# Kernel tuning notes

Hardware: AMD Instinct MI355X
Metric: run time of the kernel (lower is better)

## Reference

```python
import jax, jax.numpy as jnp
import numpy as np

M_PER_GROUP = 16
EPS = 0.001


def setup_inputs() -> dict:
    key = jax.random.key(0)
    x = jax.random.normal(key, (32, 64, 64, 256), dtype=jnp.float32)
    return {"x": x}


def reference(x) -> jnp.ndarray:
    # x: [B, W, H, C] (NHWC). Training-phase path, decomposition='cholesky', renorm=False.
    b, w, h, c = x.shape
    groups = c // M_PER_GROUP
    n = b * w * h  # samples per channel

    # [C, B*W*H]
    x_flat = jnp.transpose(x, (3, 0, 1, 2)).reshape(c, -1)
    mean = jnp.mean(x_flat, axis=1, keepdims=True)          # [C, 1]
    f = x_flat - mean                                        # [C, N]

    # per-group covariance: [G, m, N] -> [G, m, m]
    fg = f.reshape(groups, M_PER_GROUP, -1)
    denom = jnp.float32(n) - 1.0
    cov = jnp.einsum('gmn,gkn->gmk', fg, fg) / denom
    eye = jnp.eye(M_PER_GROUP, dtype=x.dtype)
    cov = (1.0 - EPS) * cov + EPS * eye
    # NOTE: the original TF code divides by (N-1) a second time after shrinkage;
    # reproduced faithfully here.
    cov = cov / denom

    # batched Cholesky + triangular solve: inv_sqrt = L^{-1}
    chol = jnp.linalg.cholesky(cov)                          # [G, m, m], lower
    inv_sqrt = jax.vmap(
        lambda L: jax.scipy.linalg.solve_triangular(L, eye, lower=True)
    )(chol)                                                  # [G, m, m]

    # whiten: [G, m, m] @ [G, m, N] -> [G, m, N]
    f_hat = jnp.einsum('gmk,gkn->gmn', inv_sqrt, fg)
    out = f_hat.reshape(c, b, w, h)
    return jnp.transpose(out, (1, 2, 3, 0))
```

## Files before the change

### kernel.cpp

```cpp
#include <hip/hip_runtime.h>


#define NROWS   131072
#define DENOMF  131071.0f
#define EPSV    0.001f

#define OFF_INV    0
#define OFF_BIAS   4096
#define OFF_RED1   4352
#define OFF_PART4  217344
#define GSTATS     13312

typedef __attribute__((ext_vector_type(8))) short bf16x8;
typedef __attribute__((ext_vector_type(4))) float f32x4;
typedef __attribute__((ext_vector_type(4))) unsigned int u32x4;

__device__ __forceinline__ unsigned int fbits(float v) {
    return __builtin_bit_cast(unsigned int, v);
}
__device__ __forceinline__ float bfloat(unsigned int u) {
    return __builtin_bit_cast(float, u);
}

struct Row8 { float a, b, c, d, e, f, g, h; };

__device__ __forceinline__ void cvt8(const Row8 r, bf16x8& hv, bf16x8& lv, float& s) {
    s += ((r.a + r.b) + (r.c + r.d)) + ((r.e + r.f) + (r.g + r.h));
    const unsigned int ua = fbits(r.a), ub = fbits(r.b), uc = fbits(r.c), ud = fbits(r.d);
    const unsigned int ue = fbits(r.e), uf = fbits(r.f), ug = fbits(r.g), uh = fbits(r.h);
    u32x4 hp;
    hp.x = (ub & 0xFFFF0000u) | (ua >> 16);
    hp.y = (ud & 0xFFFF0000u) | (uc >> 16);
    hp.z = (uf & 0xFFFF0000u) | (ue >> 16);
    hp.w = (uh & 0xFFFF0000u) | (ug >> 16);
    const float da = r.a - bfloat(ua & 0xFFFF0000u);
    const float db = r.b - bfloat(ub & 0xFFFF0000u);
    const float dc = r.c - bfloat(uc & 0xFFFF0000u);
    const float dd = r.d - bfloat(ud & 0xFFFF0000u);
    const float de = r.e - bfloat(ue & 0xFFFF0000u);
    const float df = r.f - bfloat(uf & 0xFFFF0000u);
    const float dg = r.g - bfloat(ug & 0xFFFF0000u);
    const float dh = r.h - bfloat(uh & 0xFFFF0000u);
    u32x4 lp;
    lp.x = (fbits(db) & 0xFFFF0000u) | (fbits(da) >> 16);
    lp.y = (fbits(dd) & 0xFFFF0000u) | (fbits(dc) >> 16);
    lp.z = (fbits(df) & 0xFFFF0000u) | (fbits(de) >> 16);
    lp.w = (fbits(dh) & 0xFFFF0000u) | (fbits(dg) >> 16);
    hv = __builtin_bit_cast(bf16x8, hp);
    lv = __builtin_bit_cast(bf16x8, lp);
}

__global__ __launch_bounds__(256, 2) void k1_stats(const float* __restrict__ x,
                                                   float* __restrict__ ws, int NB) {
    __shared__ float xt[32 * 260];
    const int tid = threadIdx.x;
    const int lane = tid & 63, wv = tid >> 6;
    const int slot = lane >> 4;
    const int TPB = (NROWS / 32) / NB;
    const float4* gf4 = reinterpret_cast<const float4*>(x);
    const size_t tile0 = (size_t)blockIdx.x * TPB;

    const int rb = wv * 64 + (lane & 15);
    const int ro0 = (slot * 8 + ((0 + 2 * slot) & 7)) * 260 + rb;
    const int ro1 = (slot * 8 + ((1 + 2 * slot) & 7)) * 260 + rb;
    const int ro2 = (slot * 8 + ((2 + 2 * slot) & 7)) * 260 + rb;
    const int ro3 = (slot * 8 + ((3 + 2 * slot) & 7)) * 260 + rb;
    const int ro4 = (slot * 8 + ((4 + 2 * slot) & 7)) * 260 + rb;
    const int ro5 = (slot * 8 + ((5 + 2 * slot) & 7)) * 260 + rb;
    const int ro6 = (slot * 8 + ((6 + 2 * slot) & 7)) * 260 + rb;
    const int ro7 = (slot * 8 + ((7 + 2 * slot) & 7)) * 260 + rb;

    f32x4 hh0 = {0,0,0,0}, hl0 = {0,0,0,0}, ll0 = {0,0,0,0};
    f32x4 hh1 = {0,0,0,0}, hl1 = {0,0,0,0}, ll1 = {0,0,0,0};
    f32x4 hh2 = {0,0,0,0}, hl2 = {0,0,0,0}, ll2 = {0,0,0,0};
    f32x4 hh3 = {0,0,0,0}, hl3 = {0,0,0,0}, ll3 = {0,0,0,0};
    float s0 = 0.f, s1 = 0.f, s2 = 0.f, s3 = 0.f;

    float4 st0, st1, st2, st3, st4, st5, st6, st7;
#define LOADT(T)                                                              \
    {                                                                         \
        const float4* tp = gf4 + (tile0 + (T)) * 2048 + tid;                  \
        st0 = tp[0];    st1 = tp[256];  st2 = tp[512];  st3 = tp[768];        \
        st4 = tp[1024]; st5 = tp[1280]; st6 = tp[1536]; st7 = tp[1792];       \
    }
#define WRK(K, ST)                                                            \
    {                                                                         \
        const int idx = tid + (K) * 256;                                      \
        *reinterpret_cast<float4*>(&xt[(idx >> 6) * 260 + (idx & 63) * 4]) = ST; \
    }
#define PROCG(G, AHH, AHL, ALL, S)                                            \
    {                                                                         \
        Row8 r;                                                               \
        r.a = xt[ro0 + (G) * 16]; r.b = xt[ro1 + (G) * 16];                   \
        r.c = xt[ro2 + (G) * 16]; r.d = xt[ro3 + (G) * 16];                   \
        r.e = xt[ro4 + (G) * 16]; r.f = xt[ro5 + (G) * 16];                   \
        r.g = xt[ro6 + (G) * 16]; r.h = xt[ro7 + (G) * 16];                   \
        bf16x8 hv, lv;                                                        \
        cvt8(r, hv, lv, S);                                                   \
        AHH = __builtin_amdgcn_mfma_f32_16x16x32_bf16(hv, hv, AHH, 0, 0, 0);  \
        AHL = __builtin_amdgcn_mfma_f32_16x16x32_bf16(hv, lv, AHL, 0, 0, 0);  \
        ALL = __builtin_amdgcn_mfma_f32_16x16x32_bf16(lv, lv, ALL, 0, 0, 0);  \
    }

    LOADT(0);
    for (int t = 0; t < TPB; ++t) {
        __syncthreads();
        WRK(0, st0); WRK(1, st1); WRK(2, st2); WRK(3, st3);
        WRK(4, st4); WRK(5, st5); WRK(6, st6); WRK(7, st7);
        __syncthreads();
        const int tn = (t + 1 < TPB) ? (t + 1) : t;
        LOADT(tn);
        PROCG(0, hh0, hl0, ll0, s0);
        PROCG(1, hh1, hl1, ll1, s1);
        PROCG(2, hh2, hl2, ll2, s2);
        PROCG(3, hh3, hl3, ll3, s3);
    }
#undef PROCG
#undef WRK
#undef LOADT

    float* pb = ws + OFF_PART4 + (size_t)blockIdx.x * GSTATS + (size_t)(wv * 4) * 832;
#define STG(G, AHH, AHL, ALL, S)                                              \
    {                                                                         \
        float* pw = pb + (G) * 832;                                           \
        pw[0 * 64 + lane]  = AHH[0]; pw[1 * 64 + lane]  = AHH[1];             \
        pw[2 * 64 + lane]  = AHH[2]; pw[3 * 64 + lane]  = AHH[3];             \
        pw[4 * 64 + lane]  = AHL[0]; pw[5 * 64 + lane]  = AHL[1];             \
        pw[6 * 64 + lane]  = AHL[2]; pw[7 * 64 + lane]  = AHL[3];             \
        pw[8 * 64 + lane]  = ALL[0]; pw[9 * 64 + lane]  = ALL[1];             \
        pw[10 * 64 + lane] = ALL[2]; pw[11 * 64 + lane] = ALL[3];             \
        pw[12 * 64 + lane] = S;                                               \
    }
    STG(0, hh0, hl0, ll0, s0);
    STG(1, hh1, hl1, ll1, s1);
    STG(2, hh2, hl2, ll2, s2);
    STG(3, hh3, hl3, ll3, s3);
#undef STG
}

__global__ __launch_bounds__(256, 4) void k2_reduce(float* __restrict__ ws, int NB) {
    const int t = blockIdx.x * 256 + threadIdx.x;
    if (t >= GSTATS) return;
    const int per = NB / 16;
    const float* p = ws + OFF_PART4 + (size_t)(blockIdx.y * per) * GSTATS + t;
    float sum = 0.f;
#pragma unroll 8
    for (int b = 0; b < per; ++b) sum += p[(size_t)b * GSTATS];
    ws[OFF_RED1 + (size_t)blockIdx.y * GSTATS + t] = sum;
}

__global__ void k2_chol(float* __restrict__ ws, int NB) {
    __shared__ float sg[832];
    const int g = blockIdx.x, tid = threadIdx.x;

    for (int e = tid; e < 832; e += 64) {
        float v = 0.f;
#pragma unroll
        for (int y = 0; y < 16; ++y)
            v += ws[OFF_RED1 + (size_t)y * GSTATS + g * 832 + e];
        sg[e] = v;
    }
    __syncthreads();

    const int ii = tid & 15;
    const float inv_denom = 1.0f / DENOMF;
    const float cs_ii = sg[768 + ii] + sg[768 + 16 + ii] +
                        sg[768 + 32 + ii] + sg[768 + 48 + ii];
    const float mu_l = cs_ii * (1.0f / (float)NROWS);

#define GIDX(T, I, J) ((T) * 256 + ((I) & 3) * 64 + ((((I) >> 2)) << 4) + (J))
    float arow[16];
#pragma unroll
    for (int kk = 0; kk < 16; ++kk) {
        float G = sg[GIDX(0, ii, kk)] + sg[GIDX(1, ii, kk)] +
                  sg[GIDX(1, kk, ii)] + sg[GIDX(2, ii, kk)];
        float mu_k = __shfl(mu_l, kk, 64);
        float cv = (G - (float)NROWS * mu_l * mu_k) * inv_denom;
        cv = cv * (1.0f - EPSV) + ((kk == ii) ? EPSV : 0.0f);
        arow[kk] = cv * inv_denom;
    }
#undef GIDX

    float lrow[16];
#pragma unroll
    for (int j = 0; j < 16; ++j) {
        float diag = __shfl(arow[j], j, 64);
        float ljj  = sqrtf(diag);
        float lij  = (ii == j) ? ljj : arow[j] / ljj;
        lrow[j] = lij;
#pragma unroll
        for (int k = j + 1; k < 16; ++k) {
            float lkj = __shfl(lij, k, 64);
            arow[k] = fmaf(-lij, lkj, arow[k]);
        }
    }

    float xcol[16];
#pragma unroll
    for (int i2 = 0; i2 < 16; ++i2) {
        float ssum = (ii == i2) ? 1.0f : 0.0f;
#pragma unroll
        for (int k = 0; k < 16; ++k) {
            if (k < i2) {
                float Lik = __shfl(lrow[k], i2, 64);
                ssum = fmaf(-Lik, xcol[k], ssum);
            }
        }
        float Lii = __shfl(lrow[i2], i2, 64);
        xcol[i2] = (i2 >= ii) ? ssum / Lii : 0.0f;
    }

    float* invg = ws + OFF_INV + g * 256;
#pragma unroll
    for (int i2 = 0; i2 < 16; ++i2) {
        if (tid < 16) invg[i2 * 16 + tid] = xcol[i2];
        float bi = xcol[i2] * mu_l;
        bi += __shfl_xor(bi, 1, 64);
        bi += __shfl_xor(bi, 2, 64);
        bi += __shfl_xor(bi, 4, 64);
        bi += __shfl_xor(bi, 8, 64);
        if (tid == 0) ws[OFF_BIAS + g * 16 + i2] = bi;
    }
}

template <int CTRL>
__device__ __forceinline__ float dpp1(float v) {
    int iv = __builtin_bit_cast(int, v);
    int r = __builtin_amdgcn_update_dpp(iv, iv, CTRL, 0xF, 0xF, false);
    return __builtin_bit_cast(float, r);
}
template <int CTRL>
__device__ __forceinline__ float4 dpp4(float4 v) {
    float4 r;
    r.x = dpp1<CTRL>(v.x);
    r.y = dpp1<CTRL>(v.y);
    r.z = dpp1<CTRL>(v.z);
    r.w = dpp1<CTRL>(v.w);
    return r;
}

#define DOT4(O, A, V) \
    O = fmaf(A.x, V.x, O); O = fmaf(A.y, V.y, O); \
    O = fmaf(A.z, V.z, O); O = fmaf(A.w, V.w, O)

__global__ __launch_bounds__(256, 4) void k3_apply(const float* __restrict__ x,
                                                   const float* __restrict__ ws,
                                                   float* __restrict__ out) {
    const int tid = threadIdx.x, lane = tid & 63, wv = tid >> 6;
    const int q = lane & 3, g = lane >> 2;

    const float* invg = ws + OFF_INV + g * 256;
#define LOADIR(R, M) \
    *reinterpret_cast<const float4*>(invg + (4 * q + (R)) * 16 + 4 * (q ^ (M)))
    float4 ir00 = LOADIR(0, 0), ir01 = LOADIR(0, 1), ir02 = LOADIR(0, 2), ir03 = LOADIR(0, 3);
    float4 ir10 = LOADIR(1, 0), ir11 = LOADIR(1, 1), ir12 = LOADIR(1, 2), ir13 = LOADIR(1, 3);
    float4 ir20 = LOADIR(2, 0), ir21 = LOADIR(2, 1), ir22 = LOADIR(2, 2), ir23 = LOADIR(2, 3);
    float4 ir30 = LOADIR(3, 0), ir31 = LOADIR(3, 1), ir32 = LOADIR(3, 2), ir33 = LOADIR(3, 3);
#undef LOADIR
    float4 b4 = *reinterpret_cast<const float4*>(ws + OFF_BIAS + g * 16 + 4 * q);

    const int rpb   = NROWS / gridDim.x;
    const int iters = rpb / 4;
    const size_t rowbase = (size_t)blockIdx.x * rpb;
    const float4* xp = reinterpret_cast<const float4*>(x) + rowbase * 64 + lane;
    float4*       op = reinterpret_cast<float4*>(out)     + rowbase * 64 + lane;

    float4 cur = xp[(size_t)wv * 64];
    for (int i = 0; i < iters; ++i) {
        const int ip = (i + 1 < iters) ? (i + 1) : (iters - 1);
        float4 nxt = xp[(size_t)(ip * 4 + wv) * 64];

        float4 v0 = cur;
        float4 v1 = dpp4<0xB1>(cur);
        float4 v2 = dpp4<0x4E>(cur);
        float4 v3 = dpp4<0x1B>(cur);

        float o0 = -b4.x, o1 = -b4.y, o2 = -b4.z, o3 = -b4.w;
        DOT4(o0, ir00, v0); DOT4(o0, ir01, v1); DOT4(o0, ir02, v2); DOT4(o0, ir03, v3);
        DOT4(o1, ir10, v0); DOT4(o1, ir11, v1); DOT4(o1, ir12, v2); DOT4(o1, ir13, v3);
        DOT4(o2, ir20, v0); DOT4(o2, ir21, v1); DOT4(o2, ir22, v2); DOT4(o2, ir23, v3);
        DOT4(o3, ir30, v0); DOT4(o3, ir31, v1); DOT4(o3, ir32, v2); DOT4(o3, ir33, v3);

        op[(size_t)(i * 4 + wv) * 64] = make_float4(o0, o1, o2, o3);
        cur = nxt;
    }
}

extern "C" void kernel_launch(void* const* d_in, const int* in_sizes, int n_in,
                              void* d_out, int out_size, void* d_ws, size_t ws_size,
                              hipStream_t stream) {
    const float* x = (const float*)d_in[0];
    float* out = (float*)d_out;
    float* ws  = (float*)d_ws;

    int NB = 128;
    if (ws_size >= (size_t)(OFF_PART4 + 512 * GSTATS) * sizeof(float)) NB = 512;
    else if (ws_size >= (size_t)(OFF_PART4 + 256 * GSTATS) * sizeof(float)) NB = 256;

    k1_stats<<<NB, 256, 0, stream>>>(x, ws, NB);
    dim3 rg((GSTATS + 255) / 256, 16);
    k2_reduce<<<rg, 256, 0, stream>>>(ws, NB);
    k2_chol<<<16, 64, 0, stream>>>(ws, NB);
    k3_apply<<<1024, 256, 0, stream>>>(x, ws, out);
}
```

Baseline: 98.80 us.

## Double-buffer stats tile with direct global-to-LDS async loads

The covariance-stats kernel now stages each 32-row tile straight from global memory into LDS using global_load_lds, instead of loading into registers and then writing to shared memory. The shared buffer is doubled so the next tile loads while the current one is processed, and one barrier per iteration is dropped. This aims to cut register pressure and the LDS write instructions, and to overlap memory traffic with MFMA work. It doubles the LDS footprint, which may lower occupancy. Correctness depends on the async LDS writes being complete before the barrier, and it is unclear whether the compiler inserts a wait on them before __syncthreads.

New measurement: 98.46 us. Within noise of the previous version (-0.3%).

```diff
diff --git a/kernel.cpp b/kernel.cpp
--- a/kernel.cpp
+++ b/kernel.cpp
@@ -20,6 +20,12 @@
 }
 __device__ __forceinline__ float bfloat(unsigned int u) {
     return __builtin_bit_cast(float, u);
+}
+
+__device__ __forceinline__ void gload_lds16(float* lds, const float* g) {
+    __builtin_amdgcn_global_load_lds(
+        (const __attribute__((address_space(1))) unsigned int*)g,
+        (__attribute__((address_space(3))) unsigned int*)lds, 16, 0, 0);
 }
 
 struct Row8 { float a, b, c, d, e, f, g, h; };
@@ -52,12 +58,11 @@
 
 __global__ __launch_bounds__(256, 2) void k1_stats(const float* __restrict__ x,
                                                    float* __restrict__ ws, int NB) {
-    __shared__ float xt[32 * 260];
+    __shared__ float xt[2][32 * 260];
     const int tid = threadIdx.x;
     const int lane = tid & 63, wv = tid >> 6;
     const int slot = lane >> 4;
     const int TPB = (NROWS / 32) / NB;
-    const float4* gf4 = reinterpret_cast<const float4*>(x);
     const size_t tile0 = (size_t)blockIdx.x * TPB;
 
     const int rb = wv * 64 + (lane & 15);
@@ -76,60 +81,64 @@
     f32x4 hh3 = {0,0,0,0}, hl3 = {0,0,0,0}, ll3 = {0,0,0,0};
     float s0 = 0.f, s1 = 0.f, s2 = 0.f, s3 = 0.f;
 
-    float4 st0, st1, st2, st3, st4, st5, st6, st7;
-#define LOADT(T)                                                              \
+#define STAGE(B, T)                                                           \
     {                                                                         \
-        const float4* tp = gf4 + (tile0 + (T)) * 2048 + tid;                  \
-        st0 = tp[0];    st1 = tp[256];  st2 = tp[512];  st3 = tp[768];        \
-        st4 = tp[1024]; st5 = tp[1280]; st6 = tp[1536]; st7 = tp[1792];       \
-    }
-#define WRK(K, ST)                                                            \
+        const float* gp = x + ((tile0 + (T)) * 32 + (size_t)(wv * 8)) * 256   \
+                            + (size_t)lane * 4;                               \
+        float* lb = &xt[B][(wv * 8) * 260];                                   \
+        gload_lds16(lb + 0 * 260, gp + 0 * 256);                              \
+        gload_lds16(lb + 1 * 260, gp + 1 * 256);                              \
+        gload_lds16(lb + 2 * 260, gp + 2 * 256);                              \
+        gload_lds16(lb + 3 * 260, gp + 3 * 256);                              \
+        gload_lds16(lb + 4 * 260, gp + 4 * 256);                              \
+        gload_lds16(lb + 5 * 260, gp + 5 * 256);                              \
+        gload_lds16(lb + 6 * 260, gp + 6 * 256);                              \
+        gload_lds16(lb + 7 * 260, gp + 7 * 256);                              \
+    }
+#define PROCG(B, G, AHH, AHL, ALL, S)                                         \
     {                                                                         \
-        const int idx = tid + (K) * 256;                                      \
-        *reinterpret_cast<float4*>(&xt[(idx >> 6) * 260 + (idx & 63) * 4]) = ST; \
-    }
-#define PROCG(G, AHH, AHL, ALL, S)                                            \
-    {                                                                         \
+        const float* bp = &xt[B][0];                                          \
         Row8 r;                                                               \
-        r.a = xt[ro0 + (G) * 16]; r.b = xt[ro1 + (G) * 16];                   \
-        r.c = xt[ro2 + (G) * 16]; r.d = xt[ro3 + (G) * 16];                   \
-        r.e = xt[ro4 + (G) * 16]; r.f = xt[ro5 + (G) * 16];                   \
-        r.g = xt[ro6 + (G) * 16]; r.h = xt[ro7 + (G) * 16];                   \
+        r.a = bp[ro0 + (G) * 16]; r.b = bp[ro1 + (G) * 16];                   \
+        r.c = bp[ro2 + (G) * 16]; r.d = bp[ro3 + (G) * 16];                   \
+        r.e = bp[ro4 + (G) * 16]; r.f = bp[ro5 + (G) * 16];                   \
+        r.g = bp[ro6 + (G) * 16]; r.h = bp[ro7 + (G) * 16];                   \
         bf16x8 hv, lv;                                                        \
         cvt8(r, hv, lv, S);                                                   \
         AHH = __builtin_amdgcn_mfma_f32_16x16x32_bf16(hv, hv, AHH, 0, 0, 0);  \
         AHL = __builtin_amdgcn_mfma_f32_16x16x32_bf16(hv, lv, AHL, 0, 0, 0);  \
         ALL = __builtin_amdgcn_mfma_f32_16x16x32_bf16(lv, lv, ALL, 0, 0, 0);  \
     }
-
-    LOADT(0);
-    for (int t = 0; t < TPB; ++t) {
+#define PROC4(B)                                                              \
+    PROCG(B, 0, hh0, hl0, ll0, s0);                                           \
+    PROCG(B, 1, hh1, hl1, ll1, s1);                                           \
+    PROCG(B, 2, hh2, hl2, ll2, s2);                                           \
+    PROCG(B, 3, hh3, hl3, ll3, s3);
+
+    STAGE(0, 0);
+    for (int t = 0; t < TPB - 1; ++t) {
         __syncthreads();
-        WRK(0, st0); WRK(1, st1); WRK(2, st2); WRK(3, st3);
-        WRK(4, st4); WRK(5, st5); WRK(6, st6); WRK(7, st7);
-        __syncthreads();
-        const int tn = (t + 1 < TPB) ? (t + 1) : t;
-        LOADT(tn);
-        PROCG(0, hh0, hl0, ll0, s0);
-        PROCG(1, hh1, hl1, ll1, s1);
-        PROCG(2, hh2, hl2, ll2, s2);
-        PROCG(3, hh3, hl3, ll3, s3);
-    }
+        STAGE((t + 1) & 1, t + 1);
+        PROC4(t & 1);
+    }
+    __syncthreads();
+    PROC4((TPB - 1) & 1);
+#undef PROC4
 #undef PROCG
-#undef WRK
-#undef LOADT
-
+#undef STAGE
+
+    const int lane2 = lane;
     float* pb = ws + OFF_PART4 + (size_t)blockIdx.x * GSTATS + (size_t)(wv * 4) * 832;
 #define STG(G, AHH, AHL, ALL, S)                                              \
     {                                                                         \
         float* pw = pb + (G) * 832;                                           \
-        pw[0 * 64 + lane]  = AHH[0]; pw[1 * 64 + lane]  = AHH[1];             \
-        pw[2 * 64 + lane]  = AHH[2]; pw[3 * 64 + lane]  = AHH[3];             \
-        pw[4 * 64 + lane]  = AHL[0]; pw[5 * 64 + lane]  = AHL[1];             \
-        pw[6 * 64 + lane]  = AHL[2]; pw[7 * 64 + lane]  = AHL[3];             \
-        pw[8 * 64 + lane]  = ALL[0]; pw[9 * 64 + lane]  = ALL[1];             \
-        pw[10 * 64 + lane] = ALL[2]; pw[11 * 64 + lane] = ALL[3];             \
-        pw[12 * 64 + lane] = S;                                               \
+        pw[0 * 64 + lane2]  = AHH[0]; pw[1 * 64 + lane2]  = AHH[1];           \
+        pw[2 * 64 + lane2]  = AHH[2]; pw[3 * 64 + lane2]  = AHH[3];           \
+        pw[4 * 64 + lane2]  = AHL[0]; pw[5 * 64 + lane2]  = AHL[1];           \
+        pw[6 * 64 + lane2]  = AHL[2]; pw[7 * 64 + lane2]  = AHL[3];           \
+        pw[8 * 64 + lane2]  = ALL[0]; pw[9 * 64 + lane2]  = ALL[1];           \
+        pw[10 * 64 + lane2] = ALL[2]; pw[11 * 64 + lane2] = ALL[3];           \
+        pw[12 * 64 + lane2] = S;                                              \
     }
     STG(0, hh0, hl0, ll0, s0);
     STG(1, hh1, hl1, ll1, s1);
```

## Widen stats blocks to 512 threads, fold hh+ll partials, shrink partial buffers

Applied to the files above, without the earlier changes.

The stats kernel now runs 512-thread blocks over 64-row tiles. Each wave handles two channel groups across two 32-row halves instead of four groups over one half, which halves the MFMA accumulator registers per wave. The hh and ll Gram partials are summed before they are stored, so each group's partial shrinks from 832 to 576 floats and the reduce and Cholesky kernels read less data. The maximum block count drops from 512 to 256. This trades fewer, larger blocks and lower grid parallelism for less partial-sum traffic and higher occupancy per block.

New measurement: 92.97 us. -5.9%, faster.

```diff
diff --git a/kernel.cpp b/kernel.cpp
--- a/kernel.cpp
+++ b/kernel.cpp
@@ -7,9 +7,9 @@
 
 #define OFF_INV    0
 #define OFF_BIAS   4096
-#define OFF_RED1   4352
-#define OFF_PART4  217344
-#define GSTATS     13312
+#define OFF_RED    4352
+#define OFF_PART   151808
+#define GS2        9216
 
 typedef __attribute__((ext_vector_type(8))) short bf16x8;
 typedef __attribute__((ext_vector_type(4))) float f32x4;
@@ -50,51 +50,54 @@
     lv = __builtin_bit_cast(bf16x8, lp);
 }
 
-__global__ __launch_bounds__(256, 2) void k1_stats(const float* __restrict__ x,
+__global__ __launch_bounds__(512, 4) void k1_stats(const float* __restrict__ x,
                                                    float* __restrict__ ws, int NB) {
-    __shared__ float xt[32 * 260];
+    __shared__ float xt[64 * 260];
     const int tid = threadIdx.x;
     const int lane = tid & 63, wv = tid >> 6;
     const int slot = lane >> 4;
-    const int TPB = (NROWS / 32) / NB;
+    const int TPB = (NROWS / 64) / NB;
     const float4* gf4 = reinterpret_cast<const float4*>(x);
     const size_t tile0 = (size_t)blockIdx.x * TPB;
 
-    const int rb = wv * 64 + (lane & 15);
-    const int ro0 = (slot * 8 + ((0 + 2 * slot) & 7)) * 260 + rb;
-    const int ro1 = (slot * 8 + ((1 + 2 * slot) & 7)) * 260 + rb;
-    const int ro2 = (slot * 8 + ((2 + 2 * slot) & 7)) * 260 + rb;
-    const int ro3 = (slot * 8 + ((3 + 2 * slot) & 7)) * 260 + rb;
-    const int ro4 = (slot * 8 + ((4 + 2 * slot) & 7)) * 260 + rb;
-    const int ro5 = (slot * 8 + ((5 + 2 * slot) & 7)) * 260 + rb;
-    const int ro6 = (slot * 8 + ((6 + 2 * slot) & 7)) * 260 + rb;
-    const int ro7 = (slot * 8 + ((7 + 2 * slot) & 7)) * 260 + rb;
+    const int g0 = wv * 2;
+    const int rb0 = g0 * 16 + (lane & 15);
+    const int roA0 = (0 * 32 + slot * 8 + ((0 + 2 * slot) & 7)) * 260 + rb0;
+    const int roA1 = (0 * 32 + slot * 8 + ((1 + 2 * slot) & 7)) * 260 + rb0;
+    const int roA2 = (0 * 32 + slot * 8 + ((2 + 2 * slot) & 7)) * 260 + rb0;
+    const int roA3 = (0 * 32 + slot * 8 + ((3 + 2 * slot) & 7)) * 260 + rb0;
+    const int roA4 = (0 * 32 + slot * 8 + ((4 + 2 * slot) & 7)) * 260 + rb0;
+    const int roA5 = (0 * 32 + slot * 8 + ((5 + 2 * slot) & 7)) * 260 + rb0;
+    const int roA6 = (0 * 32 + slot * 8 + ((6 + 2 * slot) & 7)) * 260 + rb0;
+    const int roA7 = (0 * 32 + slot * 8 + ((7 + 2 * slot) & 7)) * 260 + rb0;
+    const int roB0 = roA0 + 32 * 260, roB1 = roA1 + 32 * 260;
+    const int roB2 = roA2 + 32 * 260, roB3 = roA3 + 32 * 260;
+    const int roB4 = roA4 + 32 * 260, roB5 = roA5 + 32 * 260;
+    const int roB6 = roA6 + 32 * 260, roB7 = roA7 + 32 * 260;
 
     f32x4 hh0 = {0,0,0,0}, hl0 = {0,0,0,0}, ll0 = {0,0,0,0};
     f32x4 hh1 = {0,0,0,0}, hl1 = {0,0,0,0}, ll1 = {0,0,0,0};
-    f32x4 hh2 = {0,0,0,0}, hl2 = {0,0,0,0}, ll2 = {0,0,0,0};
-    f32x4 hh3 = {0,0,0,0}, hl3 = {0,0,0,0}, ll3 = {0,0,0,0};
-    float s0 = 0.f, s1 = 0.f, s2 = 0.f, s3 = 0.f;
+    float s0 = 0.f, s1 = 0.f;
 
     float4 st0, st1, st2, st3, st4, st5, st6, st7;
 #define LOADT(T)                                                              \
     {                                                                         \
-        const float4* tp = gf4 + (tile0 + (T)) * 2048 + tid;                  \
-        st0 = tp[0];    st1 = tp[256];  st2 = tp[512];  st3 = tp[768];        \
-        st4 = tp[1024]; st5 = tp[1280]; st6 = tp[1536]; st7 = tp[1792];       \
+        const float4* tp = gf4 + (tile0 + (T)) * 4096 + tid;                  \
+        st0 = tp[0];    st1 = tp[512];  st2 = tp[1024]; st3 = tp[1536];       \
+        st4 = tp[2048]; st5 = tp[2560]; st6 = tp[3072]; st7 = tp[3584];       \
     }
 #define WRK(K, ST)                                                            \
     {                                                                         \
-        const int idx = tid + (K) * 256;                                      \
+        const int idx = tid + (K) * 512;                                      \
         *reinterpret_cast<float4*>(&xt[(idx >> 6) * 260 + (idx & 63) * 4]) = ST; \
     }
-#define PROCG(G, AHH, AHL, ALL, S)                                            \
+#define PROCG(U, G, AHH, AHL, ALL, S)                                         \
     {                                                                         \
         Row8 r;                                                               \
-        r.a = xt[ro0 + (G) * 16]; r.b = xt[ro1 + (G) * 16];                   \
-        r.c = xt[ro2 + (G) * 16]; r.d = xt[ro3 + (G) * 16];                   \
-        r.e = xt[ro4 + (G) * 16]; r.f = xt[ro5 + (G) * 16];                   \
-        r.g = xt[ro6 + (G) * 16]; r.h = xt[ro7 + (G) * 16];                   \
+        r.a = xt[ro##U##0 + (G) * 16]; r.b = xt[ro##U##1 + (G) * 16];         \
+        r.c = xt[ro##U##2 + (G) * 16]; r.d = xt[ro##U##3 + (G) * 16];         \
+        r.e = xt[ro##U##4 + (G) * 16]; r.f = xt[ro##U##5 + (G) * 16];         \
+        r.g = xt[ro##U##6 + (G) * 16]; r.h = xt[ro##U##7 + (G) * 16];         \
         bf16x8 hv, lv;                                                        \
         cvt8(r, hv, lv, S);                                                   \
         AHH = __builtin_amdgcn_mfma_f32_16x16x32_bf16(hv, hv, AHH, 0, 0, 0);  \
@@ -110,76 +113,62 @@
         __syncthreads();
         const int tn = (t + 1 < TPB) ? (t + 1) : t;
         LOADT(tn);
-        PROCG(0, hh0, hl0, ll0, s0);
-        PROCG(1, hh1, hl1, ll1, s1);
-        PROCG(2, hh2, hl2, ll2, s2);
-        PROCG(3, hh3, hl3, ll3, s3);
+        PROCG(A, 0, hh0, hl0, ll0, s0);
+        PROCG(B, 0, hh0, hl0, ll0, s0);
+        PROCG(A, 1, hh1, hl1, ll1, s1);
+        PROCG(B, 1, hh1, hl1, ll1, s1);
     }
 #undef PROCG
 #undef WRK
 #undef LOADT
 
-    float* pb = ws + OFF_PART4 + (size_t)blockIdx.x * GSTATS + (size_t)(wv * 4) * 832;
+    float* pb = ws + OFF_PART + (size_t)blockIdx.x * GS2 + (size_t)g0 * 576;
 #define STG(G, AHH, AHL, ALL, S)                                              \
     {                                                                         \
-        float* pw = pb + (G) * 832;                                           \
-        pw[0 * 64 + lane]  = AHH[0]; pw[1 * 64 + lane]  = AHH[1];             \
-        pw[2 * 64 + lane]  = AHH[2]; pw[3 * 64 + lane]  = AHH[3];             \
-        pw[4 * 64 + lane]  = AHL[0]; pw[5 * 64 + lane]  = AHL[1];             \
-        pw[6 * 64 + lane]  = AHL[2]; pw[7 * 64 + lane]  = AHL[3];             \
-        pw[8 * 64 + lane]  = ALL[0]; pw[9 * 64 + lane]  = ALL[1];             \
-        pw[10 * 64 + lane] = ALL[2]; pw[11 * 64 + lane] = ALL[3];             \
-        pw[12 * 64 + lane] = S;                                               \
+        float* pw = pb + (G) * 576;                                           \
+        pw[0 * 64 + lane] = AHH[0] + ALL[0];                                  \
+        pw[1 * 64 + lane] = AHH[1] + ALL[1];                                  \
+        pw[2 * 64 + lane] = AHH[2] + ALL[2];                                  \
+        pw[3 * 64 + lane] = AHH[3] + ALL[3];                                  \
+        pw[4 * 64 + lane] = AHL[0]; pw[5 * 64 + lane] = AHL[1];               \
+        pw[6 * 64 + lane] = AHL[2]; pw[7 * 64 + lane] = AHL[3];               \
+        pw[8 * 64 + lane] = S;                                                \
     }
     STG(0, hh0, hl0, ll0, s0);
     STG(1, hh1, hl1, ll1, s1);
-    STG(2, hh2, hl2, ll2, s2);
-    STG(3, hh3, hl3, ll3, s3);
 #undef STG
 }
 
 __global__ __launch_bounds__(256, 4) void k2_reduce(float* __restrict__ ws, int NB) {
     const int t = blockIdx.x * 256 + threadIdx.x;
-    if (t >= GSTATS) return;
+    if (t >= GS2) return;
     const int per = NB / 16;
-    const float* p = ws + OFF_PART4 + (size_t)(blockIdx.y * per) * GSTATS + t;
+    const float* p = ws + OFF_PART + (size_t)(blockIdx.y * per) * GS2 + t;
     float sum = 0.f;
 #pragma unroll 8
-    for (int b = 0; b < per; ++b) sum += p[(size_t)b * GSTATS];
-    ws[OFF_RED1 + (size_t)blockIdx.y * GSTATS + t] = sum;
-}
-
-__global__ void k2_chol(float* __restrict__ ws, int NB) {
-    __shared__ float sg[832];
-    const int g = blockIdx.x, tid = threadIdx.x;
-
-    for (int e = tid; e < 832; e += 64) {
-        float v = 0.f;
-#pragma unroll
-        for (int y = 0; y < 16; ++y)
-            v += ws[OFF_RED1 + (size_t)y * GSTATS + g * 832 + e];
-        sg[e] = v;
-    }
-    __syncthreads();
-
+    for (int b = 0; b < per; ++b) sum += p[(size_t)b * GS2];
+    ws[OFF_RED + (size_t)blockIdx.y * GS2 + t] = sum;
+}
+
+__device__ __forceinline__ void chol_from_sg(const float* sg, int g, int tid,
+                                             float* __restrict__ ws) {
     const int ii = tid & 15;
     const float inv_denom = 1.0f / DENOMF;
-    const float cs_ii = sg[768 + ii] + sg[768 + 16 + ii] +
-                        sg[768 + 32 + ii] + sg[768 + 48 + ii];
+    const float cs_ii = sg[512 + ii] + sg[512 + 16 + ii] +
+                        sg[512 + 32 + ii] + sg[512 + 48 + ii];
     const float mu_l = cs_ii * (1.0f / (float)NROWS);
 
-#define GIDX(T, I, J) ((T) * 256 + ((I) & 3) * 64 + ((((I) >> 2)) << 4) + (J))
+#define GIDX2(T, I, J) ((T) * 256 + ((I) & 3) * 64 + ((((I) >> 2)) << 4) + (J))
     float arow[16];
 #pragma unroll
     for (int kk = 0; kk < 16; ++kk) {
-        float G = sg[GIDX(0, ii, kk)] + sg[GIDX(1, ii, kk)] +
-                  sg[GIDX(1, kk, ii)] + sg[GIDX(2, ii, kk)];
+        float G = sg[GIDX2(0, ii, kk)] + sg[GIDX2(1, ii, kk)] + sg[GIDX2(1, kk, ii)];
         float mu_k = __shfl(mu_l, kk, 64);
         float cv = (G - (float)NROWS * mu_l * mu_k) * inv_denom;
         cv = cv * (1.0f - EPSV) + ((kk == ii) ? EPSV : 0.0f);
         arow[kk] = cv * inv_denom;
     }
-#undef GIDX
+#undef GIDX2
 
     float lrow[16];
 #pragma unroll
@@ -221,6 +210,21 @@
         bi += __shfl_xor(bi, 8, 64);
         if (tid == 0) ws[OFF_BIAS + g * 16 + i2] = bi;
     }
+}
+
+__global__ void k2_chol(float* __restrict__ ws, int NB) {
+    __shared__ float sg[576];
+    const int g = blockIdx.x, tid = threadIdx.x;
+
+    for (int e = tid; e < 576; e += 64) {
+        float v = 0.f;
+#pragma unroll
+        for (int y = 0; y < 16; ++y)
+            v += ws[OFF_RED + (size_t)y * GS2 + g * 576 + e];
+        sg[e] = v;
+    }
+    __syncthreads();
+    chol_from_sg(sg, g, tid, ws);
 }
 
 template <int CTRL>
@@ -294,11 +298,10 @@
     float* ws  = (float*)d_ws;
 
     int NB = 128;
-    if (ws_size >= (size_t)(OFF_PART4 + 512 * GSTATS) * sizeof(float)) NB = 512;
-    else if (ws_size >= (size_t)(OFF_PART4 + 256 * GSTATS) * sizeof(float)) NB = 256;
-
-    k1_stats<<<NB, 256, 0, stream>>>(x, ws, NB);
-    dim3 rg((GSTATS + 255) / 256, 16);
+    if (ws_size >= (size_t)(OFF_PART + 256 * GS2) * sizeof(float)) NB = 256;
+
+    k1_stats<<<NB, 512, 0, stream>>>(x, ws, NB);
+    dim3 rg((GS2 + 255) / 256, 16);
     k2_reduce<<<rg, 256, 0, stream>>>(ws, NB);
     k2_chol<<<16, 64, 0, stream>>>(ws, NB);
     k3_apply<<<1024, 256, 0, stream>>>(x, ws, out);
```
